# Kernel tuning notes

Measured on AMD Instinct MI355X. Metric: run time of the kernel, lower is better.

Reference implementation:

```python
import jax, jax.numpy as jnp
import numpy as np

B, C, H, W = 8, 32, 256, 256


def setup_inputs() -> dict:
    key = jax.random.key(0)
    k1, k2, k3, k4 = jax.random.split(key, 4)
    shape = (B, C, H, W)
    x = jax.random.normal(k1, shape, dtype=jnp.float32)
    G1 = jax.random.normal(k2, shape, dtype=jnp.float32)
    G2 = jax.random.normal(k3, shape, dtype=jnp.float32)
    G3 = jax.random.normal(k4, shape, dtype=jnp.float32)
    return {"x": x, "G1": G1, "G2": G2, "G3": G3}


def _spn_forward(x, G1, G2, G3):
    # --- SpnBlock gate normalization (elementwise) ---
    sum_abs = jnp.abs(G1) + jnp.abs(G2) + jnp.abs(G3)
    sum_abs = jnp.where(sum_abs == 0, jnp.asarray(1e-6, x.dtype), sum_abs)
    mask = (sum_abs >= 1).astype(x.dtype)  # only normalize where sum(|g|) >= 1
    keep = 1.0 - mask
    G1 = keep * G1 + mask * (G1 / sum_abs)
    G2 = keep * G2 + mask * (G2 / sum_abs)
    G3 = keep * G3 + mask * (G3 / sum_abs)

    # --- GateRecurrent2dnoind (horizontal=True, reverse=False): left->right scan ---
    # h[i,j] = (1 - g1 - g2 - g3) * x[i,j] + g1*h[i-1,j-1] + g2*h[i,j-1] + g3*h[i+1,j-1]
    # Gates whose neighbor is out of range are zeroed (CUDA kernel semantics).
    Hd, Wd = x.shape[2], x.shape[3]
    row = jnp.arange(Hd)
    col_ok = (jnp.arange(Wd) > 0).astype(x.dtype)[None, None, None, :]  # no left col at j=0
    up_ok = (row > 0).astype(x.dtype)[None, None, :, None]
    dn_ok = (row < Hd - 1).astype(x.dtype)[None, None, :, None]
    g1 = G1 * col_ok * up_ok
    g2 = G2 * col_ok
    g3 = G3 * col_ok * dn_ok

    # move scan axis (W) to front: [W, B, C, H]
    xs = jnp.moveaxis(x, 3, 0)
    g1s = jnp.moveaxis(g1, 3, 0)
    g2s = jnp.moveaxis(g2, 3, 0)
    g3s = jnp.moveaxis(g3, 3, 0)

    def step(h_prev, inp):
        xj, a, b, c = inp  # each [B, C, H]
        zero = jnp.zeros_like(h_prev[..., :1])
        up = jnp.concatenate([zero, h_prev[..., :-1]], axis=-1)   # h_prev at row i-1
        dn = jnp.concatenate([h_prev[..., 1:], zero], axis=-1)    # h_prev at row i+1
        h = (1.0 - a - b - c) * xj + a * up + b * h_prev + c * dn
        return h, h

    init = jnp.zeros(x.shape[:3], dtype=x.dtype)  # [B, C, H]
    _, hs = jax.lax.scan(step, init, (xs, g1s, g2s, g3s))
    return jnp.moveaxis(hs, 0, 3)  # back to [B, C, H, W]


def reference(x, G1, G2, G3):
    return _spn_forward(x, G1, G2, G3)
```

## Files before the change

kernel.cpp:

```cpp
#include <hip/hip_runtime.h>


#define HD 256
#define WD 256
#define NS 16
#define STG 260
#define ARR_F (16 * STG)
#define STAGE_F (4 * ARR_F)
#define TILE_OFF (2 * STAGE_F)

#define F4E(v, e) ((e) == 0 ? (v).x : (e) == 1 ? (v).y : (e) == 2 ? (v).z : (v).w)

#define FENCE_BAR()                                      \
  do {                                                   \
    asm volatile("s_waitcnt lgkmcnt(0)" ::: "memory");   \
    __builtin_amdgcn_s_barrier();                        \
    asm volatile("" ::: "memory");                       \
  } while (0)

__global__ __launch_bounds__(320, 1) void spn_fwd(
    const float* __restrict__ x, const float* __restrict__ G1,
    const float* __restrict__ G2, const float* __restrict__ G3,
    float* __restrict__ out)
{
  __shared__ float lds_f[2 * STAGE_F + 16 * STG];

  const int tid = threadIdx.x;
  const int wid = tid >> 6;
  const int l   = tid & 63;
  const size_t pbase = (size_t)blockIdx.x * (HD * WD);
  const float* gp[4] = {x + pbase, G1 + pbase, G2 + pbase, G3 + pbase};
  float* op = out + pbase;

  if (wid < 4) {
    const int rq = l >> 2;
    const int cq = l & 3;
    float4 RA[4][4], RB[4][4];

    auto issueBlk = [&](float4 (&R)[4][4], int k) {
#pragma unroll
      for (int A = 0; A < 4; ++A)
#pragma unroll
        for (int i = 0; i < 4; ++i)
          R[A][i] = *(const float4*)(gp[A] +
              (size_t)(64 * wid + 16 * i + rq) * WD + 16 * k + 4 * cq);
    };

    auto normBlk = [&](float4 (&R)[4][4], int k) {
#pragma unroll
      for (int i = 0; i < 4; ++i) {
        const int row = 64 * wid + 16 * i + rq;
        const float uOk = (row > 0) ? 1.f : 0.f;
        const float dOk = (row < HD - 1) ? 1.f : 0.f;
        float nx[4], na[4], nb[4], nc[4];
#pragma unroll
        for (int e = 0; e < 4; ++e) {
          float a = F4E(R[1][i], e), b = F4E(R[2][i], e), c = F4E(R[3][i], e);
          float xx = F4E(R[0][i], e);
          float s = fabsf(a) + fabsf(b) + fabsf(c);
          float inv = (s >= 1.f) ? __builtin_amdgcn_rcpf(s) : 1.f;
          float cOk = (16 * k + 4 * cq + e > 0) ? 1.f : 0.f;
          float ga = a * inv * cOk * uOk;
          float gb = b * inv * cOk;
          float gc = c * inv * cOk * dOk;
          nx[e] = (1.f - ga - gb - gc) * xx;
          na[e] = ga; nb[e] = gb; nc[e] = gc;
        }
        R[0][i] = make_float4(nx[0], nx[1], nx[2], nx[3]);
        R[1][i] = make_float4(na[0], na[1], na[2], na[3]);
        R[2][i] = make_float4(nb[0], nb[1], nb[2], nb[3]);
        R[3][i] = make_float4(nc[0], nc[1], nc[2], nc[3]);
      }
    };

    auto writeStage = [&](float4 (&R)[4][4], float* dst) {
#pragma unroll
      for (int A = 0; A < 4; ++A)
#pragma unroll
        for (int i = 0; i < 4; ++i) {
          const int row = 64 * wid + 16 * i + rq;
#pragma unroll
          for (int e = 0; e < 4; ++e)
            dst[A * ARR_F + (4 * cq + e) * STG + row] = F4E(R[A][i], e);
        }
    };

    issueBlk(RA, 0);
    normBlk(RA, 0);
    writeStage(RA, lds_f + 0 * STAGE_F);
    issueBlk(RB, 1);
    FENCE_BAR();

#pragma unroll 1
    for (int tt = 0; tt < 8; ++tt) {
      const int t = 2 * tt;
      if (t + 2 <= 15) issueBlk(RA, t + 2);
      if (t + 1 <= 15) {
        normBlk(RB, t + 1);
        writeStage(RB, lds_f + 1 * STAGE_F);
      }
      FENCE_BAR();
      const int u = t + 1;
      if (u + 2 <= 15) issueBlk(RB, u + 2);
      if (u + 1 <= 15) {
        normBlk(RA, u + 1);
        writeStage(RA, lds_f + 0 * STAGE_F);
      }
      FENCE_BAR();
    }
  } else {
    float h[4] = {0.f, 0.f, 0.f, 0.f};
    const int cb = 4 * (l & 3);
    const int rr = l >> 2;
    float* tile = lds_f + TILE_OFF;

    FENCE_BAR();

#pragma unroll 1
    for (int t = 0; t < NS; ++t) {
      const float* src = lds_f + (t & 1) * STAGE_F;
      float4 rd[2][4];

#pragma unroll
      for (int A = 0; A < 4; ++A)
        rd[0][A] = *(const float4*)(src + A * ARR_F + 0 * STG + 4 * l);

#pragma unroll
      for (int c = 0; c < 16; ++c) {
        const int cur = c & 1, nxt = cur ^ 1;
        if (c < 15) {
#pragma unroll
          for (int A = 0; A < 4; ++A)
            rd[nxt][A] = *(const float4*)(src + A * ARR_F + (c + 1) * STG + 4 * l);
        }
        const float shU = __shfl_up(h[3], 1);
        const float shD = __shfl_down(h[0], 1);
        float hn[4];
#pragma unroll
        for (int r = 0; r < 4; ++r) {
          float up = (r == 0) ? shU : h[r - 1];
          float dn = (r == 3) ? shD : h[r + 1];
          hn[r] = fmaf(F4E(rd[cur][1], r), up,
                  fmaf(F4E(rd[cur][2], r), h[r],
                  fmaf(F4E(rd[cur][3], r), dn, F4E(rd[cur][0], r))));
        }
#pragma unroll
        for (int r = 0; r < 4; ++r) h[r] = hn[r];
        *(float4*)(tile + c * STG + 4 * l) =
            make_float4(hn[0], hn[1], hn[2], hn[3]);
      }

#pragma unroll
      for (int kk = 0; kk < 16; ++kk) {
        const int row = 16 * kk + rr;
        float4 o;
        o.x = tile[(cb + 0) * STG + row];
        o.y = tile[(cb + 1) * STG + row];
        o.z = tile[(cb + 2) * STG + row];
        o.w = tile[(cb + 3) * STG + row];
        *(float4*)(op + (size_t)row * WD + 16 * t + cb) = o;
      }
      FENCE_BAR();
    }
  }
}

extern "C" void kernel_launch(void* const* d_in, const int* in_sizes, int n_in,
                              void* d_out, int out_size, void* d_ws, size_t ws_size,
                              hipStream_t stream) {
  const float* x  = (const float*)d_in[0];
  const float* g1 = (const float*)d_in[1];
  const float* g2 = (const float*)d_in[2];
  const float* g3 = (const float*)d_in[3];
  float* outp = (float*)d_out;
  const int planes = out_size / (HD * WD);
  spn_fwd<<<planes, 320, 0, stream>>>(x, g1, g2, g3, outp);
}
```

Before: 106.2 us.

## Double producer waves and load 32-column superblocks split into two LDS slices

Raises the block from 4 to 8 producer waves (576 threads). Each producer lane now loads 32-column-wide superblocks with 8 lanes covering 128 contiguous bytes per row. Each superblock is written to LDS as two 16-column slices by alternating halves of the lanes. The intent is more memory-level parallelism and wider coalesced global reads feeding the single scan wave. In exchange it adds more barriers and register pressure, and half the lanes sit idle during each slice write.

Result: slower. 398.1 us (+274.9%).

```diff
diff --git a/kernel.cpp b/kernel.cpp
--- a/kernel.cpp
+++ b/kernel.cpp
@@ -3,7 +3,6 @@
 
 #define HD 256
 #define WD 256
-#define NS 16
 #define STG 260
 #define ARR_F (16 * STG)
 #define STAGE_F (4 * ARR_F)
@@ -18,7 +17,7 @@
     asm volatile("" ::: "memory");                       \
   } while (0)
 
-__global__ __launch_bounds__(320, 1) void spn_fwd(
+__global__ __launch_bounds__(576, 1) void spn_fwd(
     const float* __restrict__ x, const float* __restrict__ G1,
     const float* __restrict__ G2, const float* __restrict__ G3,
     float* __restrict__ out)
@@ -26,85 +25,88 @@
   __shared__ float lds_f[2 * STAGE_F + 16 * STG];
 
   const int tid = threadIdx.x;
-  const int wid = tid >> 6;
+  const int wv  = tid >> 6;
   const int l   = tid & 63;
   const size_t pbase = (size_t)blockIdx.x * (HD * WD);
   const float* gp[4] = {x + pbase, G1 + pbase, G2 + pbase, G3 + pbase};
   float* op = out + pbase;
 
-  if (wid < 4) {
-    const int rq = l >> 2;
-    const int cq = l & 3;
-    float4 RA[4][4], RB[4][4];
+  if (wv < 8) {
+    const int r8 = l >> 3;
+    const int p8 = l & 7;
+    float4 PA[4][4], PB[4][4];
 
-    auto issueBlk = [&](float4 (&R)[4][4], int k) {
+    auto burst = [&](float4 (&P)[4][4], int s) {
 #pragma unroll
       for (int A = 0; A < 4; ++A)
 #pragma unroll
         for (int i = 0; i < 4; ++i)
-          R[A][i] = *(const float4*)(gp[A] +
-              (size_t)(64 * wid + 16 * i + rq) * WD + 16 * k + 4 * cq);
+          P[A][i] = *(const float4*)(gp[A] +
+              (size_t)(32 * wv + 8 * i + r8) * WD + 32 * s + 4 * p8);
     };
 
-    auto normBlk = [&](float4 (&R)[4][4], int k) {
+    auto normSuper = [&](float4 (&P)[4][4], int s) {
 #pragma unroll
       for (int i = 0; i < 4; ++i) {
-        const int row = 64 * wid + 16 * i + rq;
+        const int row = 32 * wv + 8 * i + r8;
         const float uOk = (row > 0) ? 1.f : 0.f;
         const float dOk = (row < HD - 1) ? 1.f : 0.f;
         float nx[4], na[4], nb[4], nc[4];
 #pragma unroll
         for (int e = 0; e < 4; ++e) {
-          float a = F4E(R[1][i], e), b = F4E(R[2][i], e), c = F4E(R[3][i], e);
-          float xx = F4E(R[0][i], e);
-          float s = fabsf(a) + fabsf(b) + fabsf(c);
-          float inv = (s >= 1.f) ? __builtin_amdgcn_rcpf(s) : 1.f;
-          float cOk = (16 * k + 4 * cq + e > 0) ? 1.f : 0.f;
+          float a = F4E(P[1][i], e), b = F4E(P[2][i], e), c = F4E(P[3][i], e);
+          float xx = F4E(P[0][i], e);
+          float ssum = fabsf(a) + fabsf(b) + fabsf(c);
+          float inv = (ssum >= 1.f) ? __builtin_amdgcn_rcpf(ssum) : 1.f;
+          float cOk = (32 * s + 4 * p8 + e > 0) ? 1.f : 0.f;
           float ga = a * inv * cOk * uOk;
           float gb = b * inv * cOk;
           float gc = c * inv * cOk * dOk;
           nx[e] = (1.f - ga - gb - gc) * xx;
           na[e] = ga; nb[e] = gb; nc[e] = gc;
         }
-        R[0][i] = make_float4(nx[0], nx[1], nx[2], nx[3]);
-        R[1][i] = make_float4(na[0], na[1], na[2], na[3]);
-        R[2][i] = make_float4(nb[0], nb[1], nb[2], nb[3]);
-        R[3][i] = make_float4(nc[0], nc[1], nc[2], nc[3]);
+        P[0][i] = make_float4(nx[0], nx[1], nx[2], nx[3]);
+        P[1][i] = make_float4(na[0], na[1], na[2], na[3]);
+        P[2][i] = make_float4(nb[0], nb[1], nb[2], nb[3]);
+        P[3][i] = make_float4(nc[0], nc[1], nc[2], nc[3]);
       }
     };
 
-    auto writeStage = [&](float4 (&R)[4][4], float* dst) {
+    auto writeSlice = [&](float4 (&P)[4][4], int h, float* slot) {
+      if (((l >> 2) & 1) == h) {
+        const int c0 = (4 * p8) & 15;
 #pragma unroll
-      for (int A = 0; A < 4; ++A)
+        for (int A = 0; A < 4; ++A)
 #pragma unroll
-        for (int i = 0; i < 4; ++i) {
-          const int row = 64 * wid + 16 * i + rq;
+          for (int i = 0; i < 4; ++i) {
+            const int row = 32 * wv + 8 * i + r8;
 #pragma unroll
-          for (int e = 0; e < 4; ++e)
-            dst[A * ARR_F + (4 * cq + e) * STG + row] = F4E(R[A][i], e);
-        }
+            for (int e = 0; e < 4; ++e)
+              slot[A * ARR_F + (c0 + e) * STG + row] = F4E(P[A][i], e);
+          }
+      }
     };
 
-    issueBlk(RA, 0);
-    normBlk(RA, 0);
-    writeStage(RA, lds_f + 0 * STAGE_F);
-    issueBlk(RB, 1);
+    burst(PA, 0);
+    normSuper(PA, 0);
+    writeSlice(PA, 0, lds_f + 0 * STAGE_F);
+    burst(PB, 1);
     FENCE_BAR();
 
 #pragma unroll 1
-    for (int tt = 0; tt < 8; ++tt) {
-      const int t = 2 * tt;
-      if (t + 2 <= 15) issueBlk(RA, t + 2);
-      if (t + 1 <= 15) {
-        normBlk(RB, t + 1);
-        writeStage(RB, lds_f + 1 * STAGE_F);
-      }
+    for (int g = 0; g < 4; ++g) {
+      writeSlice(PA, 1, lds_f + 1 * STAGE_F);
       FENCE_BAR();
-      const int u = t + 1;
-      if (u + 2 <= 15) issueBlk(RB, u + 2);
-      if (u + 1 <= 15) {
-        normBlk(RA, u + 1);
-        writeStage(RA, lds_f + 0 * STAGE_F);
+      if (g < 3) burst(PA, 2 * g + 2);
+      normSuper(PB, 2 * g + 1);
+      writeSlice(PB, 0, lds_f + 0 * STAGE_F);
+      FENCE_BAR();
+      writeSlice(PB, 1, lds_f + 1 * STAGE_F);
+      FENCE_BAR();
+      if (g < 3) {
+        burst(PB, 2 * g + 3);
+        normSuper(PA, 2 * g + 2);
+        writeSlice(PA, 0, lds_f + 0 * STAGE_F);
       }
       FENCE_BAR();
     }
@@ -117,7 +119,7 @@
     FENCE_BAR();
 
 #pragma unroll 1
-    for (int t = 0; t < NS; ++t) {
+    for (int t = 0; t < 16; ++t) {
       const float* src = lds_f + (t & 1) * STAGE_F;
       float4 rd[2][4];
 
@@ -174,5 +176,5 @@
   const float* g3 = (const float*)d_in[3];
   float* outp = (float*)d_out;
   const int planes = out_size / (HD * WD);
-  spn_fwd<<<planes, 320, 0, stream>>>(x, g1, g2, g3, outp);
+  spn_fwd<<<planes, 576, 0, stream>>>(x, g1, g2, g3, outp);
 }
```
